# Performance work log

Hardware: AMD Instinct MI355X
Metric: run time of the kernel (lower is better)

## Reference

```python
import jax, jax.numpy as jnp
import numpy as np

B, T, N = 128, 4096, 48  # batch, seq_len, num NER tags


def setup_inputs() -> dict:
    key = jax.random.key(0)
    k1, k2, k3, k4, k5 = jax.random.split(key, 5)
    return {
        "emissions": jax.random.normal(k1, (B, T, N), dtype=jnp.float32) * 0.01,
        "transitions": jax.random.normal(k2, (N, N), dtype=jnp.float32) * 0.01,
        "start": jax.random.normal(k3, (N,), dtype=jnp.float32) * 0.01,
        "end": jax.random.normal(k4, (N,), dtype=jnp.float32) * 0.01,
        "tags": jax.random.randint(k5, (B, T), 0, N, dtype=jnp.int32),
    }


def _crf_nll(emissions, transitions, start, end, tags):
    # --- forward_partition: log Z via forward algorithm (logsumexp recursion) ---
    em_t = jnp.transpose(emissions, (1, 0, 2))  # [T, B, N]
    alpha0 = start[None, :] + em_t[0]           # dp[0][j] = start(j) + emit(0, j)

    def step(alpha, em):
        # alpha: [B, N] over previous tag y_; transitions[y_, y]
        new = jax.nn.logsumexp(alpha[:, :, None] + transitions[None, :, :], axis=1) + em
        return new, None

    alpha_T, _ = jax.lax.scan(step, alpha0, em_t[1:])  # [B, N]
    log_Z = jax.nn.logsumexp(alpha_T + end[None, :], axis=-1)  # [B]

    # --- score_seq: gold-path score ---
    em_score = jnp.take_along_axis(emissions, tags[:, :, None], axis=2)[:, :, 0].sum(axis=1)
    trans_score = transitions[tags[:, :-1], tags[:, 1:]].sum(axis=1)
    score = start[tags[:, 0]] + em_score + trans_score + end[tags[:, -1]]

    return log_Z - score  # per-sequence NLL, [B]


def reference(emissions, transitions, start, end, tags):
    return _crf_nll(emissions, transitions, start, end, tags)
```

## Files before the change

kernel.cpp:

```cpp
#include <hip/hip_runtime.h>
#include <cmath>

#define BB 128
#define TT 4096
#define NN 48

typedef short bf16x8 __attribute__((ext_vector_type(8)));
typedef short bf16x4 __attribute__((ext_vector_type(4)));
typedef float f32x4 __attribute__((ext_vector_type(4)));
typedef int   i32x4 __attribute__((ext_vector_type(4)));
typedef int   i32x2 __attribute__((ext_vector_type(2)));

__device__ __forceinline__ float wave_reduce_sum(float v) {
  #pragma unroll
  for (int m = 32; m >= 1; m >>= 1) v += __shfl_xor(v, m, 64);
  return v;
}
__device__ __forceinline__ float lane_bcast(float x, int lane) {
  return __uint_as_float((unsigned)__builtin_amdgcn_readlane(__float_as_int(x), lane));
}
__device__ __forceinline__ int cvt_pk_bf16(float lo, float hi) {
  int r;
  asm("v_cvt_pk_bf16_f32 %0, %1, %2" : "=v"(r) : "v"(lo), "v"(hi));
  return r;
}
__device__ __forceinline__ unsigned short f2bf(float f) {
  unsigned u = __float_as_uint(f);
  unsigned r = (u + 0x7FFFu + ((u >> 16) & 1u)) >> 16;
  return (unsigned short)r;
}

template<int NC, int CL>
__global__ __launch_bounds__(64) __attribute__((amdgpu_waves_per_eu(4, 4)))
void crf_chunk_kernel(const float* __restrict__ em,
                      const float* __restrict__ trans,
                      const int* __restrict__ tags,
                      unsigned short* __restrict__ G,
                      float* __restrict__ sc_part) {
  const int blk = blockIdx.x;
  const int b = blk / NC;
  const int c = blk % NC;
  const int l = threadIdx.x;
  const int g = l >> 4;
  const int rr = l & 15;
  const float FSCALE = 1.0f / 48.0f;

  bf16x8 Af0[3];
  bf16x4 Af1[3];
  #pragma unroll
  for (int mt = 0; mt < 3; ++mt) {
    const int i = 16 * mt + rr;
    bf16x8 a0;
    bf16x4 a1;
    #pragma unroll
    for (int e = 0; e < 8; ++e) {
      int k0 = 16 * (e >> 2) + 4 * g + (e & 3);
      a0[e] = (short)f2bf(__expf(trans[k0 * NN + i]) * FSCALE);
    }
    #pragma unroll
    for (int e = 0; e < 4; ++e) {
      int k1 = 32 + 4 * g + e;
      a1[e] = (short)f2bf(__expf(trans[k1 * NN + i]) * FSCALE);
    }
    Af0[mt] = a0; Af1[mt] = a1;
  }

  i32x4 B0s[3];
  i32x2 B1s[3];
  #pragma unroll
  for (int nt = 0; nt < 3; ++nt) {
    const int col = 16 * nt + rr;
    i32x4 b0;
    i32x2 b1;
    #pragma unroll
    for (int w = 0; w < 4; ++w) {
      int r0 = 16 * (w >> 1) + 4 * g + 2 * (w & 1);
      b0[w] = ((r0 == col) ? 0x3F80 : 0) | (((r0 + 1 == col) ? 0x3F80 : 0) << 16);
    }
    #pragma unroll
    for (int w = 0; w < 2; ++w) {
      int r0 = 32 + 4 * g + 2 * w;
      b1[w] = ((r0 == col) ? 0x3F80 : 0) | (((r0 + 1 == col) ? 0x3F80 : 0) << 16);
    }
    B0s[nt] = b0; B1s[nt] = b1;
  }

  const f32x4 zq = {0.f, 0.f, 0.f, 0.f};

  const float* embq = em + (size_t)b * TT * NN + 4 * g;
  const int t0 = c * CL + 1;

  float4 qa0, qa1, qa2, qb0, qb1, qb2;
  {
    const float* p0 = embq + (size_t)t0 * NN;
    qa0 = *(const float4*)(p0 +  0); qa1 = *(const float4*)(p0 + 16); qa2 = *(const float4*)(p0 + 32);
    qb0 = *(const float4*)(p0 + 48); qb1 = *(const float4*)(p0 + 64); qb2 = *(const float4*)(p0 + 80);
  }
  const float* pb = embq + (size_t)(t0 + 2) * NN;

  #define EXPS(Q0, Q1, Q2)                                                     \
    float w00_=__expf((Q0).x), w01_=__expf((Q0).y), w02_=__expf((Q0).z), w03_=__expf((Q0).w); \
    float w10_=__expf((Q1).x), w11_=__expf((Q1).y), w12_=__expf((Q1).z), w13_=__expf((Q1).w); \
    float w20_=__expf((Q2).x), w21_=__expf((Q2).y), w22_=__expf((Q2).z), w23_=__expf((Q2).w);

  #define BODY() do {                                                          \
    _Pragma("unroll") for (int nt = 0; nt < 3; ++nt) {                         \
      bf16x4 b1c_ = __builtin_bit_cast(bf16x4, B1s[nt]);                       \
      bf16x8 b0c_ = __builtin_bit_cast(bf16x8, B0s[nt]);                       \
      f32x4 a0_ = __builtin_amdgcn_mfma_f32_16x16x16bf16_1k(Af1[0], b1c_, zq, 0, 0, 0); \
      f32x4 a1_ = __builtin_amdgcn_mfma_f32_16x16x16bf16_1k(Af1[1], b1c_, zq, 0, 0, 0); \
      f32x4 a2_ = __builtin_amdgcn_mfma_f32_16x16x16bf16_1k(Af1[2], b1c_, zq, 0, 0, 0); \
      a0_ = __builtin_amdgcn_mfma_f32_16x16x32_bf16(Af0[0], b0c_, a0_, 0, 0, 0); \
      a1_ = __builtin_amdgcn_mfma_f32_16x16x32_bf16(Af0[1], b0c_, a1_, 0, 0, 0); \
      a2_ = __builtin_amdgcn_mfma_f32_16x16x32_bf16(Af0[2], b0c_, a2_, 0, 0, 0); \
      B0s[nt][0] = cvt_pk_bf16(a0_[0] * w00_, a0_[1] * w01_);                  \
      B0s[nt][1] = cvt_pk_bf16(a0_[2] * w02_, a0_[3] * w03_);                  \
      B0s[nt][2] = cvt_pk_bf16(a1_[0] * w10_, a1_[1] * w11_);                  \
      B0s[nt][3] = cvt_pk_bf16(a1_[2] * w12_, a1_[3] * w13_);                  \
      B1s[nt][0] = cvt_pk_bf16(a2_[0] * w20_, a2_[1] * w21_);                  \
      B1s[nt][1] = cvt_pk_bf16(a2_[2] * w22_, a2_[3] * w23_);                  \
    }                                                                          \
  } while (0)

  #define STEPF(Q0, Q1, Q2, POFF) do {                                         \
    EXPS(Q0, Q1, Q2)                                                           \
    Q0 = *(const float4*)(pb + (POFF) +  0);                                   \
    Q1 = *(const float4*)(pb + (POFF) + 16);                                   \
    Q2 = *(const float4*)(pb + (POFF) + 32);                                   \
    BODY();                                                                    \
  } while (0)

  #define STEPC(Q0, Q1, Q2, TROW) do {                                         \
    EXPS(Q0, Q1, Q2)                                                           \
    { const float* pc_ = embq + (size_t)(((TROW) > (TT - 1)) ? (TT - 1) : (TROW)) * NN; \
      Q0 = *(const float4*)(pc_ +  0);                                         \
      Q1 = *(const float4*)(pc_ + 16);                                         \
      Q2 = *(const float4*)(pc_ + 32); }                                       \
    BODY();                                                                    \
  } while (0)

  #define STEPN(Q0, Q1, Q2) do { EXPS(Q0, Q1, Q2) BODY(); } while (0)

  if (c != NC - 1) {
    #pragma unroll 1
    for (int it = 0; it < CL / 2; ++it) {
      STEPF(qa0, qa1, qa2, 0);
      STEPF(qb0, qb1, qb2, NN);
      pb += 2 * NN;
    }
  } else {
    #pragma unroll 1
    for (int it = 0; it < CL / 2 - 2; ++it) {
      STEPF(qa0, qa1, qa2, 0);
      STEPF(qb0, qb1, qb2, NN);
      pb += 2 * NN;
    }
    const int tb = t0 + CL - 4;
    STEPC(qa0, qa1, qa2, tb + 2);
    STEPC(qb0, qb1, qb2, tb + 3);
    STEPN(qa0, qa1, qa2);
  }
  #undef STEPF
  #undef STEPC
  #undef STEPN
  #undef BODY
  #undef EXPS

  unsigned short* Gc = G + (size_t)blk * (NN * NN);
  #pragma unroll
  for (int nt = 0; nt < 3; ++nt) {
    const int rowoff = (16 * nt + rr) * NN + 4 * g;
    i32x2 d0; d0[0] = B0s[nt][0]; d0[1] = B0s[nt][1];
    i32x2 d1; d1[0] = B0s[nt][2]; d1[1] = B0s[nt][3];
    i32x2 d2; d2[0] = B1s[nt][0]; d2[1] = B1s[nt][1];
    *(i32x2*)(Gc + rowoff)      = d0;
    *(i32x2*)(Gc + rowoff + 16) = d1;
    *(i32x2*)(Gc + rowoff + 32) = d2;
  }

  const int* tgb = tags + (size_t)b * TT;
  const float* emb = em + (size_t)b * TT * NN;
  float sc = 0.0f;
  const int base = c * (TT / NC);
  #pragma unroll
  for (int q = 0; q < TT / NC; q += 64) {
    int tt = base + q + l;
    int tg = tgb[tt];
    sc += emb[(size_t)tt * NN + tg];
    if (tt > 0) sc += trans[tgb[tt - 1] * NN + tg];
  }
  sc = wave_reduce_sum(sc);
  if (l == 0) sc_part[blk] = sc;
}

template<int NC>
__launch_bounds__(64, 1)
__global__ void crf_combine_kernel(const float* __restrict__ em,
                                   const float* __restrict__ startv,
                                   const float* __restrict__ endv,
                                   const int* __restrict__ tags,
                                   const unsigned short* __restrict__ G,
                                   const float* __restrict__ sc_part,
                                   float* __restrict__ out) {
  const int b = blockIdx.x;
  const int l = threadIdx.x;
  const int jc = (l < NN) ? l : (NN - 1);
  const float* emb = em + (size_t)b * TT * NN;
  const float FSCALE = 1.0f / 48.0f;

  float r = __expf(startv[jc] + emb[jc]);

  #pragma unroll 1
  for (int c = 0; c < NC; ++c) {
    const unsigned short* Gc = G + (size_t)(b * NC + c) * (NN * NN);
    float s0 = 0.f, s1 = 0.f, s2 = 0.f, s3 = 0.f;
    #pragma unroll
    for (int i = 0; i < NN; i += 4) {
      float g0 = __uint_as_float(((unsigned)Gc[(i + 0) * NN + jc]) << 16);
      float g1 = __uint_as_float(((unsigned)Gc[(i + 1) * NN + jc]) << 16);
      float g2 = __uint_as_float(((unsigned)Gc[(i + 2) * NN + jc]) << 16);
      float g3 = __uint_as_float(((unsigned)Gc[(i + 3) * NN + jc]) << 16);
      s0 = fmaf(lane_bcast(r, i + 0), g0, s0);
      s1 = fmaf(lane_bcast(r, i + 1), g1, s1);
      s2 = fmaf(lane_bcast(r, i + 2), g2, s2);
      s3 = fmaf(lane_bcast(r, i + 3), g3, s3);
    }
    r = (s0 + s1) + (s2 + s3);
  }

  float S = wave_reduce_sum((l < NN) ? r * __expf(endv[jc]) : 0.0f);
  float scp = wave_reduce_sum((l < NC) ? sc_part[b * NC + l] : 0.0f);

  if (l == 0) {
    const int* tgb = tags + (size_t)b * TT;
    double K = -log((double)FSCALE);
    double logZ = log((double)S) + 4095.0 * K;
    double score = (double)scp + (double)startv[tgb[0]] + (double)endv[tgb[TT - 1]];
    out[b] = (float)(logZ - score);
  }
}

extern "C" void kernel_launch(void* const* d_in, const int* in_sizes, int n_in,
                              void* d_out, int out_size, void* d_ws, size_t ws_size,
                              hipStream_t stream) {
  const float* em     = (const float*)d_in[0];
  const float* trans  = (const float*)d_in[1];
  const float* startv = (const float*)d_in[2];
  const float* endv   = (const float*)d_in[3];
  const int*   tags   = (const int*)d_in[4];
  float* out = (float*)d_out;

  const size_t need32 = (size_t)BB * 32 * NN * NN * 2 + (size_t)BB * 32 * 4;
  if (ws_size >= need32) {
    constexpr int NC = 32, CL = TT / 32;
    unsigned short* G = (unsigned short*)d_ws;
    float* sc_part = (float*)((char*)d_ws + (size_t)BB * NC * NN * NN * 2);
    hipLaunchKernelGGL((crf_chunk_kernel<NC, CL>), dim3(BB * NC), dim3(64), 0, stream,
                       em, trans, tags, G, sc_part);
    hipLaunchKernelGGL((crf_combine_kernel<NC>), dim3(BB), dim3(64), 0, stream,
                       em, startv, endv, tags, G, sc_part, out);
  } else {
    constexpr int NC = 16, CL = TT / 16;
    unsigned short* G = (unsigned short*)d_ws;
    float* sc_part = (float*)((char*)d_ws + (size_t)BB * NC * NN * NN * 2);
    hipLaunchKernelGGL((crf_chunk_kernel<NC, CL>), dim3(BB * NC), dim3(64), 0, stream,
                       em, trans, tags, G, sc_part);
    hipLaunchKernelGGL((crf_combine_kernel<NC>), dim3(BB), dim3(64), 0, stream,
                       em, startv, endv, tags, G, sc_part, out);
  }
}
```

Measured before the change: 151.4 us.

## Interleave two independent chunk recurrences per wave and broadcast emission weights via bpermute

Each wavefront now processes two independent time chunks (cA and cB) in lockstep, interleaving their MFMA chains so one chunk's dependent matrix multiplies can hide the latency of the other's. The grid is halved to match. Emission loading also changes: each lane loads one scalar per time step, computes a single exp, and redistributes the weights with ds_bpermute, replacing three float4 loads and twelve exps per lane. The cost is twice the register state per wave, which may reduce occupancy, plus twelve extra LDS permute operations per step.

```diff
diff --git a/kernel.cpp b/kernel.cpp
--- a/kernel.cpp
+++ b/kernel.cpp
@@ -15,6 +15,9 @@
   #pragma unroll
   for (int m = 32; m >= 1; m >>= 1) v += __shfl_xor(v, m, 64);
   return v;
+}
+__device__ __forceinline__ int bperm(int byteidx, int src) {
+  return __builtin_amdgcn_ds_bpermute(byteidx, src);
 }
 __device__ __forceinline__ float lane_bcast(float x, int lane) {
   return __uint_as_float((unsigned)__builtin_amdgcn_readlane(__float_as_int(x), lane));
@@ -37,12 +40,16 @@
                       const int* __restrict__ tags,
                       unsigned short* __restrict__ G,
                       float* __restrict__ sc_part) {
+  constexpr int NP = NC / 2;
   const int blk = blockIdx.x;
-  const int b = blk / NC;
-  const int c = blk % NC;
+  const int b = blk / NP;
+  const int q = blk % NP;
+  const int cA = q;
+  const int cB = q + NP;
   const int l = threadIdx.x;
   const int g = l >> 4;
   const int rr = l & 15;
+  const int jc = (l < NN) ? l : (NN - 1);
   const float FSCALE = 1.0f / 48.0f;
 
   bf16x8 Af0[3];
@@ -65,8 +72,8 @@
     Af0[mt] = a0; Af1[mt] = a1;
   }
 
-  i32x4 B0s[3];
-  i32x2 B1s[3];
+  i32x4 B0A[3], B0B[3];
+  i32x2 B1A[3], B1B[3];
   #pragma unroll
   for (int nt = 0; nt < 3; ++nt) {
     const int col = 16 * nt + rr;
@@ -82,115 +89,126 @@
       int r0 = 32 + 4 * g + 2 * w;
       b1[w] = ((r0 == col) ? 0x3F80 : 0) | (((r0 + 1 == col) ? 0x3F80 : 0) << 16);
     }
-    B0s[nt] = b0; B1s[nt] = b1;
+    B0A[nt] = b0; B1A[nt] = b1;
+    B0B[nt] = b0; B1B[nt] = b1;
   }
 
   const f32x4 zq = {0.f, 0.f, 0.f, 0.f};
-
-  const float* embq = em + (size_t)b * TT * NN + 4 * g;
-  const int t0 = c * CL + 1;
-
-  float4 qa0, qa1, qa2, qb0, qb1, qb2;
-  {
-    const float* p0 = embq + (size_t)t0 * NN;
-    qa0 = *(const float4*)(p0 +  0); qa1 = *(const float4*)(p0 + 16); qa2 = *(const float4*)(p0 + 32);
-    qb0 = *(const float4*)(p0 + 48); qb1 = *(const float4*)(p0 + 64); qb2 = *(const float4*)(p0 + 80);
-  }
-  const float* pb = embq + (size_t)(t0 + 2) * NN;
-
-  #define EXPS(Q0, Q1, Q2)                                                     \
-    float w00_=__expf((Q0).x), w01_=__expf((Q0).y), w02_=__expf((Q0).z), w03_=__expf((Q0).w); \
-    float w10_=__expf((Q1).x), w11_=__expf((Q1).y), w12_=__expf((Q1).z), w13_=__expf((Q1).w); \
-    float w20_=__expf((Q2).x), w21_=__expf((Q2).y), w22_=__expf((Q2).z), w23_=__expf((Q2).w);
-
-  #define BODY() do {                                                          \
-    _Pragma("unroll") for (int nt = 0; nt < 3; ++nt) {                         \
-      bf16x4 b1c_ = __builtin_bit_cast(bf16x4, B1s[nt]);                       \
-      bf16x8 b0c_ = __builtin_bit_cast(bf16x8, B0s[nt]);                       \
+  const int wbyte = g << 4;
+
+  const float* embr = em + (size_t)b * TT * NN + jc;
+  const int t0A = cA * CL + 1;
+  const int t0B = cB * CL + 1;
+
+  float pfA0 = embr[(size_t)(t0A + 0) * NN];
+  float pfA1 = embr[(size_t)(t0A + 1) * NN];
+  float pfB0 = embr[(size_t)(t0B + 0) * NN];
+  float pfB1 = embr[(size_t)(t0B + 1) * NN];
+  const float* prA = embr + (size_t)(t0A + 2) * NN;
+  const float* prB = embr + (size_t)(t0B + 2) * NN;
+
+  #define FEED(PF, LOADEXPR, WB) do {                                         \
+    float w_ = __expf(PF);                                                    \
+    PF = (LOADEXPR);                                                          \
+    int wi_ = __float_as_int(w_);                                             \
+    WB[0]  = bperm(wbyte +   0, wi_); WB[1]  = bperm(wbyte +   4, wi_);       \
+    WB[2]  = bperm(wbyte +   8, wi_); WB[3]  = bperm(wbyte +  12, wi_);       \
+    WB[4]  = bperm(wbyte +  64, wi_); WB[5]  = bperm(wbyte +  68, wi_);       \
+    WB[6]  = bperm(wbyte +  72, wi_); WB[7]  = bperm(wbyte +  76, wi_);       \
+    WB[8]  = bperm(wbyte + 128, wi_); WB[9]  = bperm(wbyte + 132, wi_);       \
+    WB[10] = bperm(wbyte + 136, wi_); WB[11] = bperm(wbyte + 140, wi_);       \
+  } while (0)
+
+  #define WF(WB, k) __uint_as_float((unsigned)WB[k])
+
+  #define COMP(WB, B0, B1) do {                                               \
+    _Pragma("unroll") for (int nt = 0; nt < 3; ++nt) {                        \
+      bf16x4 b1c_ = __builtin_bit_cast(bf16x4, B1[nt]);                       \
+      bf16x8 b0c_ = __builtin_bit_cast(bf16x8, B0[nt]);                       \
       f32x4 a0_ = __builtin_amdgcn_mfma_f32_16x16x16bf16_1k(Af1[0], b1c_, zq, 0, 0, 0); \
       f32x4 a1_ = __builtin_amdgcn_mfma_f32_16x16x16bf16_1k(Af1[1], b1c_, zq, 0, 0, 0); \
       f32x4 a2_ = __builtin_amdgcn_mfma_f32_16x16x16bf16_1k(Af1[2], b1c_, zq, 0, 0, 0); \
       a0_ = __builtin_amdgcn_mfma_f32_16x16x32_bf16(Af0[0], b0c_, a0_, 0, 0, 0); \
       a1_ = __builtin_amdgcn_mfma_f32_16x16x32_bf16(Af0[1], b0c_, a1_, 0, 0, 0); \
       a2_ = __builtin_amdgcn_mfma_f32_16x16x32_bf16(Af0[2], b0c_, a2_, 0, 0, 0); \
-      B0s[nt][0] = cvt_pk_bf16(a0_[0] * w00_, a0_[1] * w01_);                  \
-      B0s[nt][1] = cvt_pk_bf16(a0_[2] * w02_, a0_[3] * w03_);                  \
-      B0s[nt][2] = cvt_pk_bf16(a1_[0] * w10_, a1_[1] * w11_);                  \
-      B0s[nt][3] = cvt_pk_bf16(a1_[2] * w12_, a1_[3] * w13_);                  \
-      B1s[nt][0] = cvt_pk_bf16(a2_[0] * w20_, a2_[1] * w21_);                  \
-      B1s[nt][1] = cvt_pk_bf16(a2_[2] * w22_, a2_[3] * w23_);                  \
-    }                                                                          \
-  } while (0)
-
-  #define STEPF(Q0, Q1, Q2, POFF) do {                                         \
-    EXPS(Q0, Q1, Q2)                                                           \
-    Q0 = *(const float4*)(pb + (POFF) +  0);                                   \
-    Q1 = *(const float4*)(pb + (POFF) + 16);                                   \
-    Q2 = *(const float4*)(pb + (POFF) + 32);                                   \
-    BODY();                                                                    \
-  } while (0)
-
-  #define STEPC(Q0, Q1, Q2, TROW) do {                                         \
-    EXPS(Q0, Q1, Q2)                                                           \
-    { const float* pc_ = embq + (size_t)(((TROW) > (TT - 1)) ? (TT - 1) : (TROW)) * NN; \
-      Q0 = *(const float4*)(pc_ +  0);                                         \
-      Q1 = *(const float4*)(pc_ + 16);                                         \
-      Q2 = *(const float4*)(pc_ + 32); }                                       \
-    BODY();                                                                    \
-  } while (0)
-
-  #define STEPN(Q0, Q1, Q2) do { EXPS(Q0, Q1, Q2) BODY(); } while (0)
-
-  if (c != NC - 1) {
+      B0[nt][0] = cvt_pk_bf16(a0_[0] * WF(WB,0),  a0_[1] * WF(WB,1));         \
+      B0[nt][1] = cvt_pk_bf16(a0_[2] * WF(WB,2),  a0_[3] * WF(WB,3));         \
+      B0[nt][2] = cvt_pk_bf16(a1_[0] * WF(WB,4),  a1_[1] * WF(WB,5));         \
+      B0[nt][3] = cvt_pk_bf16(a1_[2] * WF(WB,6),  a1_[3] * WF(WB,7));         \
+      B1[nt][0] = cvt_pk_bf16(a2_[0] * WF(WB,8),  a2_[1] * WF(WB,9));         \
+      B1[nt][1] = cvt_pk_bf16(a2_[2] * WF(WB,10), a2_[3] * WF(WB,11));        \
+    }                                                                         \
+  } while (0)
+
+  #define PSTEP(PFA, ALOAD, PFB, BLOAD) do {                                  \
+    int wbA_[12], wbB_[12];                                                   \
+    FEED(PFA, ALOAD, wbA_);                                                   \
+    FEED(PFB, BLOAD, wbB_);                                                   \
+    COMP(wbA_, B0A, B1A);                                                     \
+    COMP(wbB_, B0B, B1B);                                                     \
+  } while (0)
+
+  if (q != NP - 1) {
     #pragma unroll 1
     for (int it = 0; it < CL / 2; ++it) {
-      STEPF(qa0, qa1, qa2, 0);
-      STEPF(qb0, qb1, qb2, NN);
-      pb += 2 * NN;
+      PSTEP(pfA0, prA[0],  pfB0, prB[0]);
+      PSTEP(pfA1, prA[NN], pfB1, prB[NN]);
+      prA += 2 * NN; prB += 2 * NN;
     }
   } else {
     #pragma unroll 1
     for (int it = 0; it < CL / 2 - 2; ++it) {
-      STEPF(qa0, qa1, qa2, 0);
-      STEPF(qb0, qb1, qb2, NN);
-      pb += 2 * NN;
-    }
-    const int tb = t0 + CL - 4;
-    STEPC(qa0, qa1, qa2, tb + 2);
-    STEPC(qb0, qb1, qb2, tb + 3);
-    STEPN(qa0, qa1, qa2);
-  }
-  #undef STEPF
-  #undef STEPC
-  #undef STEPN
-  #undef BODY
-  #undef EXPS
-
-  unsigned short* Gc = G + (size_t)blk * (NN * NN);
-  #pragma unroll
-  for (int nt = 0; nt < 3; ++nt) {
-    const int rowoff = (16 * nt + rr) * NN + 4 * g;
-    i32x2 d0; d0[0] = B0s[nt][0]; d0[1] = B0s[nt][1];
-    i32x2 d1; d1[0] = B0s[nt][2]; d1[1] = B0s[nt][3];
-    i32x2 d2; d2[0] = B1s[nt][0]; d2[1] = B1s[nt][1];
-    *(i32x2*)(Gc + rowoff)      = d0;
-    *(i32x2*)(Gc + rowoff + 16) = d1;
-    *(i32x2*)(Gc + rowoff + 32) = d2;
-  }
+      PSTEP(pfA0, prA[0],  pfB0, prB[0]);
+      PSTEP(pfA1, prA[NN], pfB1, prB[NN]);
+      prA += 2 * NN; prB += 2 * NN;
+    }
+    PSTEP(pfA0, prA[0],      pfB0, prB[0]);
+    PSTEP(pfA1, prA[NN],     pfB1, embr[(size_t)(TT-1)*NN]);
+    PSTEP(pfA0, prA[2*NN],   pfB0, embr[(size_t)(TT-1)*NN]);
+    {
+      int wbA_[12];
+      FEED(pfA1, prA[3*NN], wbA_);
+      COMP(wbA_, B0A, B1A);
+    }
+  }
+  #undef PSTEP
+  #undef COMP
+  #undef WF
+  #undef FEED
+
+  #define STOREG(CIDX, B0, B1) do {                                           \
+    unsigned short* Gc_ = G + (size_t)(b * NC + (CIDX)) * (NN * NN);          \
+    _Pragma("unroll") for (int nt = 0; nt < 3; ++nt) {                        \
+      const int rowoff = (16 * nt + rr) * NN + 4 * g;                         \
+      i32x2 d0; d0[0] = B0[nt][0]; d0[1] = B0[nt][1];                         \
+      i32x2 d1; d1[0] = B0[nt][2]; d1[1] = B0[nt][3];                         \
+      i32x2 d2; d2[0] = B1[nt][0]; d2[1] = B1[nt][1];                         \
+      *(i32x2*)(Gc_ + rowoff)      = d0;                                      \
+      *(i32x2*)(Gc_ + rowoff + 16) = d1;                                      \
+      *(i32x2*)(Gc_ + rowoff + 32) = d2;                                      \
+    }                                                                         \
+  } while (0)
+  STOREG(cA, B0A, B1A);
+  STOREG(cB, B0B, B1B);
+  #undef STOREG
 
   const int* tgb = tags + (size_t)b * TT;
   const float* emb = em + (size_t)b * TT * NN;
-  float sc = 0.0f;
-  const int base = c * (TT / NC);
-  #pragma unroll
-  for (int q = 0; q < TT / NC; q += 64) {
-    int tt = base + q + l;
-    int tg = tgb[tt];
-    sc += emb[(size_t)tt * NN + tg];
-    if (tt > 0) sc += trans[tgb[tt - 1] * NN + tg];
-  }
-  sc = wave_reduce_sum(sc);
-  if (l == 0) sc_part[blk] = sc;
+  #pragma unroll
+  for (int s = 0; s < 2; ++s) {
+    const int c = s ? cB : cA;
+    float sc = 0.0f;
+    const int base = c * (TT / NC);
+    #pragma unroll
+    for (int qq = 0; qq < TT / NC; qq += 64) {
+      int tt = base + qq + l;
+      int tg = tgb[tt];
+      sc += emb[(size_t)tt * NN + tg];
+      if (tt > 0) sc += trans[tgb[tt - 1] * NN + tg];
+    }
+    sc = wave_reduce_sum(sc);
+    if (l == 0) sc_part[b * NC + c] = sc;
+  }
 }
 
 template<int NC>
@@ -255,7 +273,7 @@
     constexpr int NC = 32, CL = TT / 32;
     unsigned short* G = (unsigned short*)d_ws;
     float* sc_part = (float*)((char*)d_ws + (size_t)BB * NC * NN * NN * 2);
-    hipLaunchKernelGGL((crf_chunk_kernel<NC, CL>), dim3(BB * NC), dim3(64), 0, stream,
+    hipLaunchKernelGGL((crf_chunk_kernel<NC, CL>), dim3(BB * NC / 2), dim3(64), 0, stream,
                        em, trans, tags, G, sc_part);
     hipLaunchKernelGGL((crf_combine_kernel<NC>), dim3(BB), dim3(64), 0, stream,
                        em, startv, endv, tags, G, sc_part, out);
@@ -263,7 +281,7 @@
     constexpr int NC = 16, CL = TT / 16;
     unsigned short* G = (unsigned short*)d_ws;
     float* sc_part = (float*)((char*)d_ws + (size_t)BB * NC * NN * NN * 2);
-    hipLaunchKernelGGL((crf_chunk_kernel<NC, CL>), dim3(BB * NC), dim3(64), 0, stream,
+    hipLaunchKernelGGL((crf_chunk_kernel<NC, CL>), dim3(BB * NC / 2), dim3(64), 0, stream,
                        em, trans, tags, G, sc_part);
     hipLaunchKernelGGL((crf_combine_kernel<NC>), dim3(BB), dim3(64), 0, stream,
                        em, startv, endv, tags, G, sc_part, out);
```

New measurement: 141.9 us. 1.07x faster.

## Stage exponentiated emissions as bf16 in LDS per 64-row batch

Applied to the files above, without the earlier changes.

Each block now loads 64 emission rows cooperatively with coalesced loads, applies exp once per element, packs the results to bf16 and stores them in shared memory. The recurrence steps then read packed weights from LDS instead of issuing float4 global loads and 12 redundant exps per lane. This removes the duplicated transcendental work and the global-load latency from the serial MFMA chain. The trade-offs are a barrier-separated staging phase with no overlap, and weights rounded to bf16. The chunk loop is also hardcoded to 128 rows, which breaks the NC=16 fallback path.

```diff
diff --git a/kernel.cpp b/kernel.cpp
--- a/kernel.cpp
+++ b/kernel.cpp
@@ -45,6 +45,8 @@
   const int rr = l & 15;
   const float FSCALE = 1.0f / 48.0f;
 
+  __shared__ unsigned int Wlds[64 * 24];
+
   bf16x8 Af0[3];
   bf16x4 Af1[3];
   #pragma unroll
@@ -87,84 +89,71 @@
 
   const f32x4 zq = {0.f, 0.f, 0.f, 0.f};
 
-  const float* embq = em + (size_t)b * TT * NN + 4 * g;
   const int t0 = c * CL + 1;
-
-  float4 qa0, qa1, qa2, qb0, qb1, qb2;
-  {
-    const float* p0 = embq + (size_t)t0 * NN;
-    qa0 = *(const float4*)(p0 +  0); qa1 = *(const float4*)(p0 + 16); qa2 = *(const float4*)(p0 + 32);
-    qb0 = *(const float4*)(p0 + 48); qb1 = *(const float4*)(p0 + 64); qb2 = *(const float4*)(p0 + 80);
-  }
-  const float* pb = embq + (size_t)(t0 + 2) * NN;
-
-  #define EXPS(Q0, Q1, Q2)                                                     \
-    float w00_=__expf((Q0).x), w01_=__expf((Q0).y), w02_=__expf((Q0).z), w03_=__expf((Q0).w); \
-    float w10_=__expf((Q1).x), w11_=__expf((Q1).y), w12_=__expf((Q1).z), w13_=__expf((Q1).w); \
-    float w20_=__expf((Q2).x), w21_=__expf((Q2).y), w22_=__expf((Q2).z), w23_=__expf((Q2).w);
-
-  #define BODY() do {                                                          \
-    _Pragma("unroll") for (int nt = 0; nt < 3; ++nt) {                         \
-      bf16x4 b1c_ = __builtin_bit_cast(bf16x4, B1s[nt]);                       \
-      bf16x8 b0c_ = __builtin_bit_cast(bf16x8, B0s[nt]);                       \
+  const float* emb = em + (size_t)b * TT * NN;
+
+  #define U2F(x) __uint_as_float(x)
+
+  #define STEP(S) do {                                                        \
+    const unsigned int* wrow_ = &Wlds[(S) * 24 + 2 * g];                      \
+    unsigned int q0x_ = wrow_[0],  q0y_ = wrow_[1];                           \
+    unsigned int q1x_ = wrow_[8],  q1y_ = wrow_[9];                           \
+    unsigned int q2x_ = wrow_[16], q2y_ = wrow_[17];                          \
+    float wb_[12];                                                            \
+    wb_[0]  = U2F(q0x_ << 16); wb_[1]  = U2F(q0x_ & 0xFFFF0000u);             \
+    wb_[2]  = U2F(q0y_ << 16); wb_[3]  = U2F(q0y_ & 0xFFFF0000u);             \
+    wb_[4]  = U2F(q1x_ << 16); wb_[5]  = U2F(q1x_ & 0xFFFF0000u);             \
+    wb_[6]  = U2F(q1y_ << 16); wb_[7]  = U2F(q1y_ & 0xFFFF0000u);             \
+    wb_[8]  = U2F(q2x_ << 16); wb_[9]  = U2F(q2x_ & 0xFFFF0000u);             \
+    wb_[10] = U2F(q2y_ << 16); wb_[11] = U2F(q2y_ & 0xFFFF0000u);             \
+    _Pragma("unroll") for (int nt = 0; nt < 3; ++nt) {                        \
+      bf16x4 b1c_ = __builtin_bit_cast(bf16x4, B1s[nt]);                      \
+      bf16x8 b0c_ = __builtin_bit_cast(bf16x8, B0s[nt]);                      \
       f32x4 a0_ = __builtin_amdgcn_mfma_f32_16x16x16bf16_1k(Af1[0], b1c_, zq, 0, 0, 0); \
       f32x4 a1_ = __builtin_amdgcn_mfma_f32_16x16x16bf16_1k(Af1[1], b1c_, zq, 0, 0, 0); \
       f32x4 a2_ = __builtin_amdgcn_mfma_f32_16x16x16bf16_1k(Af1[2], b1c_, zq, 0, 0, 0); \
       a0_ = __builtin_amdgcn_mfma_f32_16x16x32_bf16(Af0[0], b0c_, a0_, 0, 0, 0); \
       a1_ = __builtin_amdgcn_mfma_f32_16x16x32_bf16(Af0[1], b0c_, a1_, 0, 0, 0); \
       a2_ = __builtin_amdgcn_mfma_f32_16x16x32_bf16(Af0[2], b0c_, a2_, 0, 0, 0); \
-      B0s[nt][0] = cvt_pk_bf16(a0_[0] * w00_, a0_[1] * w01_);                  \
-      B0s[nt][1] = cvt_pk_bf16(a0_[2] * w02_, a0_[3] * w03_);                  \
-      B0s[nt][2] = cvt_pk_bf16(a1_[0] * w10_, a1_[1] * w11_);                  \
-      B0s[nt][3] = cvt_pk_bf16(a1_[2] * w12_, a1_[3] * w13_);                  \
-      B1s[nt][0] = cvt_pk_bf16(a2_[0] * w20_, a2_[1] * w21_);                  \
-      B1s[nt][1] = cvt_pk_bf16(a2_[2] * w22_, a2_[3] * w23_);                  \
-    }                                                                          \
+      B0s[nt][0] = cvt_pk_bf16(a0_[0] * wb_[0],  a0_[1] * wb_[1]);            \
+      B0s[nt][1] = cvt_pk_bf16(a0_[2] * wb_[2],  a0_[3] * wb_[3]);            \
+      B0s[nt][2] = cvt_pk_bf16(a1_[0] * wb_[4],  a1_[1] * wb_[5]);            \
+      B0s[nt][3] = cvt_pk_bf16(a1_[2] * wb_[6],  a1_[3] * wb_[7]);            \
+      B1s[nt][0] = cvt_pk_bf16(a2_[0] * wb_[8],  a2_[1] * wb_[9]);            \
+      B1s[nt][1] = cvt_pk_bf16(a2_[2] * wb_[10], a2_[3] * wb_[11]);           \
+    }                                                                         \
   } while (0)
 
-  #define STEPF(Q0, Q1, Q2, POFF) do {                                         \
-    EXPS(Q0, Q1, Q2)                                                           \
-    Q0 = *(const float4*)(pb + (POFF) +  0);                                   \
-    Q1 = *(const float4*)(pb + (POFF) + 16);                                   \
-    Q2 = *(const float4*)(pb + (POFF) + 32);                                   \
-    BODY();                                                                    \
-  } while (0)
-
-  #define STEPC(Q0, Q1, Q2, TROW) do {                                         \
-    EXPS(Q0, Q1, Q2)                                                           \
-    { const float* pc_ = embq + (size_t)(((TROW) > (TT - 1)) ? (TT - 1) : (TROW)) * NN; \
-      Q0 = *(const float4*)(pc_ +  0);                                         \
-      Q1 = *(const float4*)(pc_ + 16);                                         \
-      Q2 = *(const float4*)(pc_ + 32); }                                       \
-    BODY();                                                                    \
-  } while (0)
-
-  #define STEPN(Q0, Q1, Q2) do { EXPS(Q0, Q1, Q2) BODY(); } while (0)
-
-  if (c != NC - 1) {
+  #pragma unroll 1
+  for (int h = 0; h < 2; ++h) {
+    const int rowbase = t0 + 64 * h;
+    const int nrows = (c == NC - 1 && h == 1) ? 63 : 64;
+
+    __syncthreads();
+    {
+      const float* src = emb + (size_t)rowbase * NN;
+      const int maxfi = nrows * NN - 2;
+      #pragma unroll 4
+      for (int it = 0; it < 24; ++it) {
+        int p = it * 64 + l;
+        int fi = 2 * p;
+        fi = (fi > maxfi) ? maxfi : fi;
+        float2 v = *(const float2*)(src + fi);
+        Wlds[p] = (unsigned)cvt_pk_bf16(__expf(v.x), __expf(v.y));
+      }
+    }
+    __syncthreads();
+
     #pragma unroll 1
-    for (int it = 0; it < CL / 2; ++it) {
-      STEPF(qa0, qa1, qa2, 0);
-      STEPF(qb0, qb1, qb2, NN);
-      pb += 2 * NN;
-    }
-  } else {
-    #pragma unroll 1
-    for (int it = 0; it < CL / 2 - 2; ++it) {
-      STEPF(qa0, qa1, qa2, 0);
-      STEPF(qb0, qb1, qb2, NN);
-      pb += 2 * NN;
-    }
-    const int tb = t0 + CL - 4;
-    STEPC(qa0, qa1, qa2, tb + 2);
-    STEPC(qb0, qb1, qb2, tb + 3);
-    STEPN(qa0, qa1, qa2);
-  }
-  #undef STEPF
-  #undef STEPC
-  #undef STEPN
-  #undef BODY
-  #undef EXPS
+    for (int s = 0; s < nrows; s += 4) {
+      STEP(s + 0);
+      STEP(s + 1);
+      STEP(s + 2);
+      if (s + 3 < nrows) STEP(s + 3);
+    }
+  }
+  #undef STEP
+  #undef U2F
 
   unsigned short* Gc = G + (size_t)blk * (NN * NN);
   #pragma unroll
@@ -179,7 +168,6 @@
   }
 
   const int* tgb = tags + (size_t)b * TT;
-  const float* emb = em + (size_t)b * TT * NN;
   float sc = 0.0f;
   const int base = c * (TT / NC);
   #pragma unroll
@@ -250,7 +238,7 @@
   const int*   tags   = (const int*)d_in[4];
   float* out = (float*)d_out;
 
-  const size_t need32 = (size_t)BB * 32 * NN * NN * 2 + (size_t)BB * 32 * 4;
+  const size_t need32 = (size_t)BB * 32 * (NN * NN * 2 + 4);
   if (ws_size >= need32) {
     constexpr int NC = 32, CL = TT / 32;
     unsigned short* G = (unsigned short*)d_ws;
```

Measured after the change: 125.3 us. 1.21x faster.
